# Performance work log

Measured on AMD Instinct MI355X. Metric: run time of the kernel, lower is better.

Reference implementation:

```python
import jax, jax.numpy as jnp
import numpy as np

B, D, H, W = 16, 512, 64, 64
K = 64  # clusters
EPS = 1e-12  # torch F.normalize eps


def _l2norm(v, axis):
    n = jnp.linalg.norm(v, axis=axis, keepdims=True)
    return v / jnp.maximum(n, EPS)


def setup_inputs() -> dict:
    key = jax.random.key(0)
    k1, k2, k3, k4 = jax.random.split(key, 4)
    x = jax.random.normal(k1, (B, D, H, W), dtype=jnp.float32)
    # conv weight/bias are independent trainable params after init; sample them
    centers = jax.random.uniform(k2, (K, D), dtype=jnp.float32)
    conv_w = 2.0 * 100.0 * centers + 0.01 * jax.random.normal(k3, (K, D), dtype=jnp.float32)
    conv_b = -100.0 * jnp.linalg.norm(centers, axis=1) + 0.01 * jax.random.normal(k4, (K,), dtype=jnp.float32)
    return {"x": x, "conv_w": conv_w, "conv_b": conv_b, "centers": centers}


def reference(x, conv_w, conv_b, centers):
    b = x.shape[0]
    x_flat = x.reshape(b, D, -1)                       # (B, D, N)
    # 1x1 conv == per-location linear over channels
    logits = jnp.einsum('bdn,kd->bkn', x_flat, conv_w) + conv_b[None, :, None]
    w = jax.nn.softmax(logits, axis=1)                 # softmax over clusters
    # vlad[b,k,d] = sum_n w[b,k,n]*(x[b,d,n] - c[k,d])
    #            = (w @ x^T)[b,k,d] - (sum_n w[b,k,n]) * c[k,d]
    wx = jnp.einsum('bkn,bdn->bkd', w, x_flat)         # (B, K, D)
    wsum = jnp.sum(w, axis=-1)                          # (B, K)
    vlad = wx - wsum[:, :, None] * centers[None]        # (B, K, D)
    vlad = _l2norm(vlad, axis=2)                        # intra-normalize
    vlad = vlad.reshape(b, -1)
    vlad = _l2norm(vlad, axis=1)                        # global L2
    return vlad
```

## Files before the change

### kernel.cpp

```cpp
#include <hip/hip_runtime.h>
#include <hip/hip_bf16.h>
#include <math.h>

#define B_ 16
#define D_ 512
#define N_ 4096
#define K_ 64

typedef __attribute__((ext_vector_type(8))) short bfrag;
typedef __attribute__((ext_vector_type(4))) float f32x4;

static __device__ __forceinline__ float bf2f(unsigned short u) {
    return __uint_as_float(((unsigned)u) << 16);
}
static __device__ __forceinline__ unsigned short f2bf(float v) {
    __hip_bfloat16 h = __float2bfloat16(v);
    union { __hip_bfloat16 h; unsigned short u; } cv; cv.h = h; return cv.u;
}
static __device__ __forceinline__ void split3(float v, unsigned short& h,
                                              unsigned short& m, unsigned short& l) {
    h = f2bf(v); float r1 = v - bf2f(h);
    m = f2bf(r1); float r2 = r1 - bf2f(m);
    l = f2bf(r2);
}
static __device__ __forceinline__ void split2(float v, unsigned short& h,
                                              unsigned short& l) {
    h = f2bf(v); l = f2bf(v - bf2f(h));
}
#define MFMA(a, b, c) __builtin_amdgcn_mfma_f32_16x16x32_bf16((a), (b), (c), 0, 0, 0)

static __device__ __forceinline__ int xf_idx(int row, int col) {
    const int CH  = col >> 2;
    const int CHs = ((CH - 2 * (row & 7)) & 7) | (CH & 8);
    return row * 68 + CHs * 4 + (col & 3);
}
static __device__ __forceinline__ int ws_idx(int k, int n) {
    const int CH  = n >> 3;
    const int CHs = (CH - 2 * (k & 7)) & 7;
    return k * 72 + CHs * 8 + (n & 7);
}

__global__ __launch_bounds__(256) void k_prep(
    const float* __restrict__ conv_w, unsigned short* __restrict__ cwL)
{
    const int i = blockIdx.x * 256 + threadIdx.x;
    const float4 v = *(const float4*)&conv_w[i * 4];
    const float vv[4] = {v.x, v.y, v.z, v.w};
    unsigned short h[4], m[4], l[4];
    #pragma unroll
    for (int j = 0; j < 4; ++j) split3(vv[j], h[j], m[j], l[j]);
    *(ushort4*)&cwL[0 * (K_ * D_) + i * 4] = make_ushort4(h[0], h[1], h[2], h[3]);
    *(ushort4*)&cwL[1 * (K_ * D_) + i * 4] = make_ushort4(m[0], m[1], m[2], m[3]);
    *(ushort4*)&cwL[2 * (K_ * D_) + i * 4] = make_ushort4(l[0], l[1], l[2], l[3]);
}

__global__ __launch_bounds__(512, 2) void k_fused(
    const float* __restrict__ x, const unsigned short* __restrict__ cwL,
    const float* __restrict__ conv_b, float* __restrict__ vlad_part,
    float* __restrict__ wsumbuf)
{
    const int b    = blockIdx.x >> 4;
    const int g    = blockIdx.x & 15;
    const int tid  = threadIdx.x;
    const int w    = tid >> 6;
    const int lane = tid & 63;
    const int q    = lane >> 4;
    const int c    = lane & 15;
    const int kw   = w >> 1;
    const int nw   = w & 1;
    const int dsub = w * 4;

    extern __shared__ char smem[];
    float*          xf   = (float*)smem;
    unsigned short* xsb  = (unsigned short*)(smem + 139264);
    unsigned short* wsb_ = (unsigned short*)(smem + 139264);
    float*          redm = (float*)(smem + 157696);
    float*          reds = (float*)(smem + 158720);

    f32x4 acc2[16];
    #pragma unroll
    for (int i = 0; i < 16; ++i) acc2[i] = (f32x4){0.f, 0.f, 0.f, 0.f};
    float wacc[4] = {0.f, 0.f, 0.f, 0.f};
    float bias[4];
    #pragma unroll
    for (int r = 0; r < 4; ++r) bias[r] = conv_b[kw * 16 + q * 4 + r];

    const unsigned short* cwp = cwL + (kw * 16 + c) * D_ + q * 8;

    #pragma unroll 1
    for (int t = 0; t < 4; ++t) {
        const int gn0 = g * 256 + t * 64;
        const float* xb = x + (size_t)b * ((size_t)D_ * N_) + gn0 + lane;

        f32x4 accA[2];
        accA[0] = (f32x4){0.f, 0.f, 0.f, 0.f};
        accA[1] = (f32x4){0.f, 0.f, 0.f, 0.f};

        float gx[4];
        #pragma unroll
        for (int r = 0; r < 4; ++r) gx[r] = xb[(size_t)(dsub + r) * N_];

        #pragma unroll 1
        for (int d0 = 0; d0 < D_; d0 += 32) {
            const bfrag af0 = *(const bfrag*)(cwp + d0);
            const bfrag af1 = *(const bfrag*)(cwp + K_ * D_ + d0);
            const bfrag af2 = *(const bfrag*)(cwp + 2 * K_ * D_ + d0);
            const int dn = (d0 + 32) & (D_ - 1);
            float nx[4];
            #pragma unroll
            for (int r = 0; r < 4; ++r) nx[r] = xb[(size_t)(dn + dsub + r) * N_];

            #pragma unroll
            for (int r = 0; r < 4; ++r) xf[xf_idx(d0 + dsub + r, lane)] = gx[r];
            unsigned short h[4], m[4], l[4];
            #pragma unroll
            for (int r = 0; r < 4; ++r) split3(gx[r], h[r], m[r], l[r]);
            {
                const int Cs  = (dsub >> 3) ^ ((lane >> 3) & 3);
                const int dsw = Cs * 8 + (dsub & 7);
                *(ushort4*)&xsb[0 * 2560 + lane * 40 + dsw] = make_ushort4(h[0], h[1], h[2], h[3]);
                *(ushort4*)&xsb[1 * 2560 + lane * 40 + dsw] = make_ushort4(m[0], m[1], m[2], m[3]);
                *(ushort4*)&xsb[2 * 2560 + lane * 40 + dsw] = make_ushort4(l[0], l[1], l[2], l[3]);
            }
            __syncthreads();
            #pragma unroll
            for (int nt = 0; nt < 2; ++nt) {
                const int row = nw * 32 + nt * 16 + c;
                const int qs  = (q ^ ((row >> 3) & 3)) * 8;
                const bfrag bf0 = *(const bfrag*)&xsb[0 * 2560 + row * 40 + qs];
                const bfrag bf1 = *(const bfrag*)&xsb[1 * 2560 + row * 40 + qs];
                const bfrag bf2 = *(const bfrag*)&xsb[2 * 2560 + row * 40 + qs];
                f32x4 a = accA[nt];
                a = MFMA(af0, bf0, a);
                a = MFMA(af0, bf1, a);
                a = MFMA(af1, bf0, a);
                a = MFMA(af1, bf1, a);
                a = MFMA(af0, bf2, a);
                a = MFMA(af2, bf0, a);
                accA[nt] = a;
            }
            __syncthreads();
            #pragma unroll
            for (int r = 0; r < 4; ++r) gx[r] = nx[r];
        }

        #pragma unroll
        for (int nt = 0; nt < 2; ++nt)
            #pragma unroll
            for (int r = 0; r < 4; ++r) accA[nt][r] += bias[r];

        {
            float ml[2];
            #pragma unroll
            for (int nt = 0; nt < 2; ++nt) {
                float mm = fmaxf(fmaxf(accA[nt][0], accA[nt][1]),
                                 fmaxf(accA[nt][2], accA[nt][3]));
                mm = fmaxf(mm, __shfl_xor(mm, 16));
                mm = fmaxf(mm, __shfl_xor(mm, 32));
                ml[nt] = mm;
            }
            if (q == 0) {
                redm[kw * 64 + nw * 32 + c]      = ml[0];
                redm[kw * 64 + nw * 32 + 16 + c] = ml[1];
            }
        }
        __syncthreads();
        float mall[2];
        #pragma unroll
        for (int nt = 0; nt < 2; ++nt) {
            const int n = nw * 32 + nt * 16 + c;
            mall[nt] = fmaxf(fmaxf(redm[n], redm[64 + n]),
                             fmaxf(redm[128 + n], redm[192 + n]));
        }
        float sl[2] = {0.f, 0.f};
        #pragma unroll
        for (int nt = 0; nt < 2; ++nt) {
            #pragma unroll
            for (int r = 0; r < 4; ++r) {
                const float e = __expf(accA[nt][r] - mall[nt]);
                accA[nt][r] = e;
                sl[nt] += e;
            }
            sl[nt] += __shfl_xor(sl[nt], 16);
            sl[nt] += __shfl_xor(sl[nt], 32);
        }
        if (q == 0) {
            reds[kw * 64 + nw * 32 + c]      = sl[0];
            reds[kw * 64 + nw * 32 + 16 + c] = sl[1];
        }
        __syncthreads();
        #pragma unroll
        for (int nt = 0; nt < 2; ++nt) {
            const int n = nw * 32 + nt * 16 + c;
            const float inv = 1.0f / (reds[n] + reds[64 + n] + reds[128 + n] + reds[192 + n]);
            #pragma unroll
            for (int r = 0; r < 4; ++r) {
                const float v = accA[nt][r] * inv;
                unsigned short hi, lo;
                split2(v, hi, lo);
                const int k = kw * 16 + q * 4 + r;
                wsb_[ws_idx(k, n)]        = hi;
                wsb_[4608 + ws_idx(k, n)] = lo;
                wacc[r] += v;
            }
        }
        __syncthreads();

        bfrag awh[2], awl[2];
        #pragma unroll
        for (int ns = 0; ns < 2; ++ns) {
            awh[ns] = *(const bfrag*)&wsb_[ws_idx(kw * 16 + c, ns * 32 + q * 8)];
            awl[ns] = *(const bfrag*)&wsb_[4608 + ws_idx(kw * 16 + c, ns * 32 + q * 8)];
        }
        #pragma unroll
        for (int i = 0; i < 16; ++i) {
            const int row = i * 32 + nw * 16 + c;
            f32x4 a = acc2[i];
            #pragma unroll
            for (int ns = 0; ns < 2; ++ns) {
                const float4 v0 = *(const float4*)&xf[xf_idx(row, ns * 32 + q * 8)];
                const float4 v1 = *(const float4*)&xf[xf_idx(row, ns * 32 + q * 8 + 4)];
                const float vv[8] = {v0.x, v0.y, v0.z, v0.w, v1.x, v1.y, v1.z, v1.w};
                bfrag bh, bl;
                #pragma unroll
                for (int j = 0; j < 8; ++j) {
                    unsigned short hh, ll;
                    split2(vv[j], hh, ll);
                    bh[j] = (short)hh;
                    bl[j] = (short)ll;
                }
                a = MFMA(awh[ns], bh, a);
                a = MFMA(awh[ns], bl, a);
                a = MFMA(awl[ns], bh, a);
            }
            acc2[i] = a;
        }
        __syncthreads();
    }

    #pragma unroll
    for (int msk = 1; msk < 16; msk <<= 1)
        #pragma unroll
        for (int r = 0; r < 4; ++r) wacc[r] += __shfl_xor(wacc[r], msk);
    if (c == 0)
        #pragma unroll
        for (int r = 0; r < 4; ++r)
            atomicAdd(&wsumbuf[b * K_ + kw * 16 + q * 4 + r], wacc[r]);

    float* vp = vlad_part + ((size_t)(b * 16 + g) * K_) * D_;
    #pragma unroll
    for (int i = 0; i < 16; ++i)
        #pragma unroll
        for (int r = 0; r < 4; ++r)
            vp[(size_t)(kw * 16 + q * 4 + r) * D_ + i * 32 + nw * 16 + c] = acc2[i][r];
}

__global__ __launch_bounds__(256) void k_norm(
    const float* __restrict__ wsumbuf, const float* __restrict__ vlad_part,
    const float* __restrict__ centers, float* __restrict__ out)
{
    const int b   = blockIdx.x >> 6;
    const int k   = blockIdx.x & 63;
    const int tid = threadIdx.x;

    const float wsum = wsumbuf[b * K_ + k];

    const float* vp = vlad_part + ((size_t)(b * 16) * K_ + k) * D_;
    float a0 = 0.f, a1 = 0.f;
    #pragma unroll 4
    for (int gg = 0; gg < 16; ++gg) {
        a0 += vp[(size_t)gg * K_ * D_ + tid];
        a1 += vp[(size_t)gg * K_ * D_ + tid + 256];
    }
    const float* cr = centers + k * D_;
    const float v0 = a0 - wsum * cr[tid];
    const float v1 = a1 - wsum * cr[tid + 256];

    float ss = v0 * v0 + v1 * v1;
    __shared__ float red2[4];
    #pragma unroll
    for (int off = 32; off > 0; off >>= 1) ss += __shfl_down(ss, off, 64);
    if ((tid & 63) == 0) red2[tid >> 6] = ss;
    __syncthreads();
    const float nrm = sqrtf(red2[0] + red2[1] + red2[2] + red2[3]);
    const float scale = 1.0f / (8.0f * fmaxf(nrm, 1e-12f));

    float* outr = out + ((size_t)b * K_ + k) * D_;
    outr[tid]       = v0 * scale;
    outr[tid + 256] = v1 * scale;
}

extern "C" void kernel_launch(void* const* d_in, const int* in_sizes, int n_in,
                              void* d_out, int out_size, void* d_ws, size_t ws_size,
                              hipStream_t stream) {
    const float* x       = (const float*)d_in[0];
    const float* conv_w  = (const float*)d_in[1];
    const float* conv_b  = (const float*)d_in[2];
    const float* centers = (const float*)d_in[3];
    float* out = (float*)d_out;

    char* wsp = (char*)d_ws;
    float* vlad_part    = (float*)wsp;
    float* wsumbuf      = (float*)(wsp + (32u << 20));
    unsigned short* cwL = (unsigned short*)(wsp + (32u << 20) + (1u << 16));

    hipMemsetAsync(wsumbuf, 0, B_ * K_ * sizeof(float), stream);

    static bool attr_set = false;
    if (!attr_set) {
        (void)hipFuncSetAttribute((const void*)k_fused,
                                  hipFuncAttributeMaxDynamicSharedMemorySize, 159744);
        attr_set = true;
    }

    k_prep<<<32, 256, 0, stream>>>(conv_w, cwL);
    k_fused<<<B_ * 16, 512, 159744, stream>>>(x, cwL, conv_b, vlad_part, wsumbuf);
    k_norm<<<B_ * K_, 256, 0, stream>>>(wsumbuf, vlad_part, centers, out);
}
```

Before: 257.1 us.

## Halve per-block N tile to double grid size and cut shared memory

Each fused block now handles 128 spatial positions instead of 256, processed in 32-wide chunks, so the grid doubles to 512 blocks and shared memory per block roughly halves. The logits GEMM now steps over 64 channels per iteration, and the LDS layouts and swizzles are rebuilt for the smaller tile. This targets poor CU fill, since 256 blocks cannot cover the machine well, and raises the occupancy hint. The cost is twice as many partial VLAD slabs to write and reduce in the norm kernel, plus more workspace.

After: 352.4 us. 37.1% more time.

```diff
diff --git a/kernel.cpp b/kernel.cpp
--- a/kernel.cpp
+++ b/kernel.cpp
@@ -29,15 +29,8 @@
 }
 #define MFMA(a, b, c) __builtin_amdgcn_mfma_f32_16x16x32_bf16((a), (b), (c), 0, 0, 0)
 
-static __device__ __forceinline__ int xf_idx(int row, int col) {
-    const int CH  = col >> 2;
-    const int CHs = ((CH - 2 * (row & 7)) & 7) | (CH & 8);
-    return row * 68 + CHs * 4 + (col & 3);
-}
-static __device__ __forceinline__ int ws_idx(int k, int n) {
-    const int CH  = n >> 3;
-    const int CHs = (CH - 2 * (k & 7)) & 7;
-    return k * 72 + CHs * 8 + (n & 7);
+static __device__ __forceinline__ int xf_idx(int d, int n) {
+    return d * 32 + ((((n >> 2) - d) & 7) << 2) + (n & 3);
 }
 
 __global__ __launch_bounds__(256) void k_prep(
@@ -54,28 +47,29 @@
     *(ushort4*)&cwL[2 * (K_ * D_) + i * 4] = make_ushort4(l[0], l[1], l[2], l[3]);
 }
 
-__global__ __launch_bounds__(512, 2) void k_fused(
+__global__ __launch_bounds__(512, 4) void k_fused(
     const float* __restrict__ x, const unsigned short* __restrict__ cwL,
     const float* __restrict__ conv_b, float* __restrict__ vlad_part,
     float* __restrict__ wsumbuf)
 {
-    const int b    = blockIdx.x >> 4;
-    const int g    = blockIdx.x & 15;
+    const int b    = blockIdx.x >> 5;
+    const int g    = blockIdx.x & 31;
     const int tid  = threadIdx.x;
     const int w    = tid >> 6;
     const int lane = tid & 63;
     const int q    = lane >> 4;
     const int c    = lane & 15;
     const int kw   = w >> 1;
-    const int nw   = w & 1;
-    const int dsub = w * 4;
+    const int nh   = w & 1;
+    const int sn   = tid & 31;
+    const int sg   = tid >> 5;
 
     extern __shared__ char smem[];
     float*          xf   = (float*)smem;
-    unsigned short* xsb  = (unsigned short*)(smem + 139264);
-    unsigned short* wsb_ = (unsigned short*)(smem + 139264);
-    float*          redm = (float*)(smem + 157696);
-    float*          reds = (float*)(smem + 158720);
+    unsigned short* xsb  = (unsigned short*)(smem + 65536);
+    unsigned short* wsb  = (unsigned short*)(smem + 65536);
+    float*          redm = (float*)(smem + 75776);
+    float*          reds = (float*)(smem + 76288);
 
     f32x4 acc2[16];
     #pragma unroll
@@ -86,58 +80,56 @@
     for (int r = 0; r < 4; ++r) bias[r] = conv_b[kw * 16 + q * 4 + r];
 
     const unsigned short* cwp = cwL + (kw * 16 + c) * D_ + q * 8;
+    const int nloc = nh * 16 + c;
 
     #pragma unroll 1
     for (int t = 0; t < 4; ++t) {
-        const int gn0 = g * 256 + t * 64;
-        const float* xb = x + (size_t)b * ((size_t)D_ * N_) + gn0 + lane;
-
-        f32x4 accA[2];
-        accA[0] = (f32x4){0.f, 0.f, 0.f, 0.f};
-        accA[1] = (f32x4){0.f, 0.f, 0.f, 0.f};
+        const float* xb = x + (size_t)b * ((size_t)D_ * N_) + (g * 128 + t * 32) + sn;
+
+        f32x4 accA = (f32x4){0.f, 0.f, 0.f, 0.f};
 
         float gx[4];
         #pragma unroll
-        for (int r = 0; r < 4; ++r) gx[r] = xb[(size_t)(dsub + r) * N_];
+        for (int r = 0; r < 4; ++r) gx[r] = xb[(size_t)(sg * 4 + r) * N_];
 
         #pragma unroll 1
-        for (int d0 = 0; d0 < D_; d0 += 32) {
-            const bfrag af0 = *(const bfrag*)(cwp + d0);
-            const bfrag af1 = *(const bfrag*)(cwp + K_ * D_ + d0);
-            const bfrag af2 = *(const bfrag*)(cwp + 2 * K_ * D_ + d0);
-            const int dn = (d0 + 32) & (D_ - 1);
+        for (int d0 = 0; d0 < D_; d0 += 64) {
+            bfrag af[2][3];
+            #pragma unroll
+            for (int h = 0; h < 2; ++h)
+                #pragma unroll
+                for (int lv = 0; lv < 3; ++lv)
+                    af[h][lv] = *(const bfrag*)(cwp + lv * (K_ * D_) + d0 + h * 32);
+            const int dn = (d0 + 64) & (D_ - 1);
             float nx[4];
             #pragma unroll
-            for (int r = 0; r < 4; ++r) nx[r] = xb[(size_t)(dn + dsub + r) * N_];
-
-            #pragma unroll
-            for (int r = 0; r < 4; ++r) xf[xf_idx(d0 + dsub + r, lane)] = gx[r];
-            unsigned short h[4], m[4], l[4];
-            #pragma unroll
-            for (int r = 0; r < 4; ++r) split3(gx[r], h[r], m[r], l[r]);
+            for (int r = 0; r < 4; ++r) nx[r] = xb[(size_t)(dn + sg * 4 + r) * N_];
+
+            unsigned short h4[4], m4[4], l4[4];
+            #pragma unroll
+            for (int r = 0; r < 4; ++r) {
+                xf[xf_idx(d0 + sg * 4 + r, sn)] = gx[r];
+                split3(gx[r], h4[r], m4[r], l4[r]);
+            }
             {
-                const int Cs  = (dsub >> 3) ^ ((lane >> 3) & 3);
-                const int dsw = Cs * 8 + (dsub & 7);
-                *(ushort4*)&xsb[0 * 2560 + lane * 40 + dsw] = make_ushort4(h[0], h[1], h[2], h[3]);
-                *(ushort4*)&xsb[1 * 2560 + lane * 40 + dsw] = make_ushort4(m[0], m[1], m[2], m[3]);
-                *(ushort4*)&xsb[2 * 2560 + lane * 40 + dsw] = make_ushort4(l[0], l[1], l[2], l[3]);
+                const int o = sn * 72 + sg * 4;
+                *(ushort4*)&xsb[o]        = make_ushort4(h4[0], h4[1], h4[2], h4[3]);
+                *(ushort4*)&xsb[2304 + o] = make_ushort4(m4[0], m4[1], m4[2], m4[3]);
+                *(ushort4*)&xsb[4608 + o] = make_ushort4(l4[0], l4[1], l4[2], l4[3]);
             }
             __syncthreads();
             #pragma unroll
-            for (int nt = 0; nt < 2; ++nt) {
-                const int row = nw * 32 + nt * 16 + c;
-                const int qs  = (q ^ ((row >> 3) & 3)) * 8;
-                const bfrag bf0 = *(const bfrag*)&xsb[0 * 2560 + row * 40 + qs];
-                const bfrag bf1 = *(const bfrag*)&xsb[1 * 2560 + row * 40 + qs];
-                const bfrag bf2 = *(const bfrag*)&xsb[2 * 2560 + row * 40 + qs];
-                f32x4 a = accA[nt];
-                a = MFMA(af0, bf0, a);
-                a = MFMA(af0, bf1, a);
-                a = MFMA(af1, bf0, a);
-                a = MFMA(af1, bf1, a);
-                a = MFMA(af0, bf2, a);
-                a = MFMA(af2, bf0, a);
-                accA[nt] = a;
+            for (int h = 0; h < 2; ++h) {
+                const int ro = nloc * 72 + h * 32 + q * 8;
+                const bfrag bf0 = *(const bfrag*)&xsb[ro];
+                const bfrag bf1 = *(const bfrag*)&xsb[2304 + ro];
+                const bfrag bf2 = *(const bfrag*)&xsb[4608 + ro];
+                accA = MFMA(af[h][0], bf0, accA);
+                accA = MFMA(af[h][0], bf1, accA);
+                accA = MFMA(af[h][1], bf0, accA);
+                accA = MFMA(af[h][1], bf1, accA);
+                accA = MFMA(af[h][0], bf2, accA);
+                accA = MFMA(af[h][2], bf0, accA);
             }
             __syncthreads();
             #pragma unroll
@@ -145,94 +137,61 @@
         }
 
         #pragma unroll
-        for (int nt = 0; nt < 2; ++nt)
-            #pragma unroll
-            for (int r = 0; r < 4; ++r) accA[nt][r] += bias[r];
-
-        {
-            float ml[2];
-            #pragma unroll
-            for (int nt = 0; nt < 2; ++nt) {
-                float mm = fmaxf(fmaxf(accA[nt][0], accA[nt][1]),
-                                 fmaxf(accA[nt][2], accA[nt][3]));
-                mm = fmaxf(mm, __shfl_xor(mm, 16));
-                mm = fmaxf(mm, __shfl_xor(mm, 32));
-                ml[nt] = mm;
-            }
-            if (q == 0) {
-                redm[kw * 64 + nw * 32 + c]      = ml[0];
-                redm[kw * 64 + nw * 32 + 16 + c] = ml[1];
-            }
-        }
-        __syncthreads();
-        float mall[2];
-        #pragma unroll
-        for (int nt = 0; nt < 2; ++nt) {
-            const int n = nw * 32 + nt * 16 + c;
-            mall[nt] = fmaxf(fmaxf(redm[n], redm[64 + n]),
-                             fmaxf(redm[128 + n], redm[192 + n]));
-        }
-        float sl[2] = {0.f, 0.f};
-        #pragma unroll
-        for (int nt = 0; nt < 2; ++nt) {
-            #pragma unroll
-            for (int r = 0; r < 4; ++r) {
-                const float e = __expf(accA[nt][r] - mall[nt]);
-                accA[nt][r] = e;
-                sl[nt] += e;
-            }
-            sl[nt] += __shfl_xor(sl[nt], 16);
-            sl[nt] += __shfl_xor(sl[nt], 32);
-        }
-        if (q == 0) {
-            reds[kw * 64 + nw * 32 + c]      = sl[0];
-            reds[kw * 64 + nw * 32 + 16 + c] = sl[1];
-        }
-        __syncthreads();
-        #pragma unroll
-        for (int nt = 0; nt < 2; ++nt) {
-            const int n = nw * 32 + nt * 16 + c;
-            const float inv = 1.0f / (reds[n] + reds[64 + n] + reds[128 + n] + reds[192 + n]);
-            #pragma unroll
-            for (int r = 0; r < 4; ++r) {
-                const float v = accA[nt][r] * inv;
-                unsigned short hi, lo;
-                split2(v, hi, lo);
-                const int k = kw * 16 + q * 4 + r;
-                wsb_[ws_idx(k, n)]        = hi;
-                wsb_[4608 + ws_idx(k, n)] = lo;
-                wacc[r] += v;
-            }
-        }
-        __syncthreads();
-
-        bfrag awh[2], awl[2];
-        #pragma unroll
-        for (int ns = 0; ns < 2; ++ns) {
-            awh[ns] = *(const bfrag*)&wsb_[ws_idx(kw * 16 + c, ns * 32 + q * 8)];
-            awl[ns] = *(const bfrag*)&wsb_[4608 + ws_idx(kw * 16 + c, ns * 32 + q * 8)];
-        }
+        for (int r = 0; r < 4; ++r) accA[r] += bias[r];
+
+        float mm = fmaxf(fmaxf(accA[0], accA[1]), fmaxf(accA[2], accA[3]));
+        mm = fmaxf(mm, __shfl_xor(mm, 16));
+        mm = fmaxf(mm, __shfl_xor(mm, 32));
+        if (q == 0) redm[kw * 32 + nloc] = mm;
+        __syncthreads();
+        const float mall = fmaxf(fmaxf(redm[nloc], redm[32 + nloc]),
+                                 fmaxf(redm[64 + nloc], redm[96 + nloc]));
+        float sl = 0.f;
+        #pragma unroll
+        for (int r = 0; r < 4; ++r) {
+            const float e = __expf(accA[r] - mall);
+            accA[r] = e;
+            sl += e;
+        }
+        sl += __shfl_xor(sl, 16);
+        sl += __shfl_xor(sl, 32);
+        if (q == 0) reds[kw * 32 + nloc] = sl;
+        __syncthreads();
+        const float inv = 1.0f / (reds[nloc] + reds[32 + nloc] +
+                                  reds[64 + nloc] + reds[96 + nloc]);
+        #pragma unroll
+        for (int r = 0; r < 4; ++r) {
+            const float v = accA[r] * inv;
+            unsigned short hi, lo;
+            split2(v, hi, lo);
+            const int k = kw * 16 + q * 4 + r;
+            wsb[k * 40 + nloc]        = hi;
+            wsb[2560 + k * 40 + nloc] = lo;
+            wacc[r] += v;
+        }
+        __syncthreads();
+
+        const bfrag awh = *(const bfrag*)&wsb[(kw * 16 + c) * 40 + q * 8];
+        const bfrag awl = *(const bfrag*)&wsb[2560 + (kw * 16 + c) * 40 + q * 8];
         #pragma unroll
         for (int i = 0; i < 16; ++i) {
-            const int row = i * 32 + nw * 16 + c;
+            const int row = i * 32 + nh * 16 + c;
+            const int rb  = row * 32;
+            const float4 v0 = *(const float4*)&xf[rb + (((2 * q     - row) & 7) << 2)];
+            const float4 v1 = *(const float4*)&xf[rb + (((2 * q + 1 - row) & 7) << 2)];
+            const float vv[8] = {v0.x, v0.y, v0.z, v0.w, v1.x, v1.y, v1.z, v1.w};
+            bfrag bh, bl;
+            #pragma unroll
+            for (int j = 0; j < 8; ++j) {
+                unsigned short hh, ll;
+                split2(vv[j], hh, ll);
+                bh[j] = (short)hh;
+                bl[j] = (short)ll;
+            }
             f32x4 a = acc2[i];
-            #pragma unroll
-            for (int ns = 0; ns < 2; ++ns) {
-                const float4 v0 = *(const float4*)&xf[xf_idx(row, ns * 32 + q * 8)];
-                const float4 v1 = *(const float4*)&xf[xf_idx(row, ns * 32 + q * 8 + 4)];
-                const float vv[8] = {v0.x, v0.y, v0.z, v0.w, v1.x, v1.y, v1.z, v1.w};
-                bfrag bh, bl;
-                #pragma unroll
-                for (int j = 0; j < 8; ++j) {
-                    unsigned short hh, ll;
-                    split2(vv[j], hh, ll);
-                    bh[j] = (short)hh;
-                    bl[j] = (short)ll;
-                }
-                a = MFMA(awh[ns], bh, a);
-                a = MFMA(awh[ns], bl, a);
-                a = MFMA(awl[ns], bh, a);
-            }
+            a = MFMA(awh, bh, a);
+            a = MFMA(awh, bl, a);
+            a = MFMA(awl, bh, a);
             acc2[i] = a;
         }
         __syncthreads();
@@ -247,12 +206,12 @@
         for (int r = 0; r < 4; ++r)
             atomicAdd(&wsumbuf[b * K_ + kw * 16 + q * 4 + r], wacc[r]);
 
-    float* vp = vlad_part + ((size_t)(b * 16 + g) * K_) * D_;
+    float* vp = vlad_part + ((size_t)(b * 32 + g) * K_) * D_;
     #pragma unroll
     for (int i = 0; i < 16; ++i)
         #pragma unroll
         for (int r = 0; r < 4; ++r)
-            vp[(size_t)(kw * 16 + q * 4 + r) * D_ + i * 32 + nw * 16 + c] = acc2[i][r];
+            vp[(size_t)(kw * 16 + q * 4 + r) * D_ + i * 32 + nh * 16 + c] = acc2[i][r];
 }
 
 __global__ __launch_bounds__(256) void k_norm(
@@ -265,10 +224,10 @@
 
     const float wsum = wsumbuf[b * K_ + k];
 
-    const float* vp = vlad_part + ((size_t)(b * 16) * K_ + k) * D_;
+    const float* vp = vlad_part + ((size_t)(b * 32) * K_ + k) * D_;
     float a0 = 0.f, a1 = 0.f;
     #pragma unroll 4
-    for (int gg = 0; gg < 16; ++gg) {
+    for (int gg = 0; gg < 32; ++gg) {
         a0 += vp[(size_t)gg * K_ * D_ + tid];
         a1 += vp[(size_t)gg * K_ * D_ + tid + 256];
     }
@@ -301,19 +260,19 @@
 
     char* wsp = (char*)d_ws;
     float* vlad_part    = (float*)wsp;
-    float* wsumbuf      = (float*)(wsp + (32u << 20));
-    unsigned short* cwL = (unsigned short*)(wsp + (32u << 20) + (1u << 16));
+    float* wsumbuf      = (float*)(wsp + (64u << 20));
+    unsigned short* cwL = (unsigned short*)(wsp + (64u << 20) + (1u << 16));
 
     hipMemsetAsync(wsumbuf, 0, B_ * K_ * sizeof(float), stream);
 
     static bool attr_set = false;
     if (!attr_set) {
         (void)hipFuncSetAttribute((const void*)k_fused,
-                                  hipFuncAttributeMaxDynamicSharedMemorySize, 159744);
+                                  hipFuncAttributeMaxDynamicSharedMemorySize, 79360);
         attr_set = true;
     }
 
     k_prep<<<32, 256, 0, stream>>>(conv_w, cwL);
-    k_fused<<<B_ * 16, 512, 159744, stream>>>(x, cwL, conv_b, vlad_part, wsumbuf);
+    k_fused<<<B_ * 32, 512, 79360, stream>>>(x, cwL, conv_b, vlad_part, wsumbuf);
     k_norm<<<B_ * K_, 256, 0, stream>>>(wsumbuf, vlad_part, centers, out);
 }
```

## Store pre-split bf16 x tiles in LDS and software-pipeline the logits loop

Applied to the files above, without the earlier changes.

The fp32 x tile kept in shared memory is replaced by pre-split bf16 high and middle planes, written during the logits pass. The second GEMM now loads ready bfrag operands instead of re-reading fp32 and re-splitting. The logits loop is fully unrolled with double-buffered weight fragments and a 3-deep prefetch of x. __syncthreads is replaced by explicit lgkmcnt waits plus raw s_barrier with sched_barriers. The intent is to cut VALU split work and LDS traffic and to hide global latency, at the cost of more registers and a new unswizzled LDS layout that may cause bank conflicts.

After: 307.7 us. 19.7% more time.

```diff
diff --git a/kernel.cpp b/kernel.cpp
--- a/kernel.cpp
+++ b/kernel.cpp
@@ -29,11 +29,6 @@
 }
 #define MFMA(a, b, c) __builtin_amdgcn_mfma_f32_16x16x32_bf16((a), (b), (c), 0, 0, 0)
 
-static __device__ __forceinline__ int xf_idx(int row, int col) {
-    const int CH  = col >> 2;
-    const int CHs = ((CH - 2 * (row & 7)) & 7) | (CH & 8);
-    return row * 68 + CHs * 4 + (col & 3);
-}
 static __device__ __forceinline__ int ws_idx(int k, int n) {
     const int CH  = n >> 3;
     const int CHs = (CH - 2 * (k & 7)) & 7;
@@ -71,9 +66,10 @@
     const int dsub = w * 4;
 
     extern __shared__ char smem[];
-    float*          xf   = (float*)smem;
+    unsigned short* Lh   = (unsigned short*)smem;
+    unsigned short* Lm   = (unsigned short*)(smem + 69632);
     unsigned short* xsb  = (unsigned short*)(smem + 139264);
-    unsigned short* wsb_ = (unsigned short*)(smem + 139264);
+    unsigned short* wsb  = (unsigned short*)(smem + 139264);
     float*          redm = (float*)(smem + 157696);
     float*          reds = (float*)(smem + 158720);
 
@@ -96,33 +92,50 @@
         accA[0] = (f32x4){0.f, 0.f, 0.f, 0.f};
         accA[1] = (f32x4){0.f, 0.f, 0.f, 0.f};
 
-        float gx[4];
-        #pragma unroll
-        for (int r = 0; r < 4; ++r) gx[r] = xb[(size_t)(dsub + r) * N_];
-
-        #pragma unroll 1
-        for (int d0 = 0; d0 < D_; d0 += 32) {
-            const bfrag af0 = *(const bfrag*)(cwp + d0);
-            const bfrag af1 = *(const bfrag*)(cwp + K_ * D_ + d0);
-            const bfrag af2 = *(const bfrag*)(cwp + 2 * K_ * D_ + d0);
-            const int dn = (d0 + 32) & (D_ - 1);
-            float nx[4];
-            #pragma unroll
-            for (int r = 0; r < 4; ++r) nx[r] = xb[(size_t)(dn + dsub + r) * N_];
-
-            #pragma unroll
-            for (int r = 0; r < 4; ++r) xf[xf_idx(d0 + dsub + r, lane)] = gx[r];
-            unsigned short h[4], m[4], l[4];
-            #pragma unroll
-            for (int r = 0; r < 4; ++r) split3(gx[r], h[r], m[r], l[r]);
+        float gxb[3][4];
+        bfrag afb[2][3];
+
+        #pragma unroll
+        for (int r = 0; r < 4; ++r) gxb[0][r] = xb[(size_t)(dsub + r) * N_];
+        #pragma unroll
+        for (int lv = 0; lv < 3; ++lv)
+            afb[0][lv] = *(const bfrag*)(cwp + lv * (K_ * D_));
+        #pragma unroll
+        for (int r = 0; r < 4; ++r) gxb[1][r] = xb[(size_t)(32 + dsub + r) * N_];
+
+        #pragma unroll
+        for (int s = 0; s < 16; ++s) {
+            const int d0 = s * 32;
+            if (s < 15) {
+                #pragma unroll
+                for (int lv = 0; lv < 3; ++lv)
+                    afb[(s + 1) & 1][lv] =
+                        *(const bfrag*)(cwp + lv * (K_ * D_) + (s + 1) * 32);
+            }
+            if (s < 14) {
+                #pragma unroll
+                for (int r = 0; r < 4; ++r)
+                    gxb[(s + 2) % 3][r] =
+                        xb[(size_t)((s + 2) * 32 + dsub + r) * N_];
+            }
+            unsigned short h4[4], m4[4], l4[4];
+            #pragma unroll
+            for (int r = 0; r < 4; ++r) {
+                split3(gxb[s % 3][r], h4[r], m4[r], l4[r]);
+                Lh[(d0 + dsub + r) * 68 + lane] = h4[r];
+                Lm[(d0 + dsub + r) * 68 + lane] = m4[r];
+            }
             {
                 const int Cs  = (dsub >> 3) ^ ((lane >> 3) & 3);
                 const int dsw = Cs * 8 + (dsub & 7);
-                *(ushort4*)&xsb[0 * 2560 + lane * 40 + dsw] = make_ushort4(h[0], h[1], h[2], h[3]);
-                *(ushort4*)&xsb[1 * 2560 + lane * 40 + dsw] = make_ushort4(m[0], m[1], m[2], m[3]);
-                *(ushort4*)&xsb[2 * 2560 + lane * 40 + dsw] = make_ushort4(l[0], l[1], l[2], l[3]);
-            }
-            __syncthreads();
+                *(ushort4*)&xsb[0 * 2560 + lane * 40 + dsw] = make_ushort4(h4[0], h4[1], h4[2], h4[3]);
+                *(ushort4*)&xsb[1 * 2560 + lane * 40 + dsw] = make_ushort4(m4[0], m4[1], m4[2], m4[3]);
+                *(ushort4*)&xsb[2 * 2560 + lane * 40 + dsw] = make_ushort4(l4[0], l4[1], l4[2], l4[3]);
+            }
+            asm volatile("s_waitcnt lgkmcnt(0)" ::: "memory");
+            __builtin_amdgcn_sched_barrier(0);
+            __builtin_amdgcn_s_barrier();
+            __builtin_amdgcn_sched_barrier(0);
             #pragma unroll
             for (int nt = 0; nt < 2; ++nt) {
                 const int row = nw * 32 + nt * 16 + c;
@@ -131,17 +144,18 @@
                 const bfrag bf1 = *(const bfrag*)&xsb[1 * 2560 + row * 40 + qs];
                 const bfrag bf2 = *(const bfrag*)&xsb[2 * 2560 + row * 40 + qs];
                 f32x4 a = accA[nt];
-                a = MFMA(af0, bf0, a);
-                a = MFMA(af0, bf1, a);
-                a = MFMA(af1, bf0, a);
-                a = MFMA(af1, bf1, a);
-                a = MFMA(af0, bf2, a);
-                a = MFMA(af2, bf0, a);
+                a = MFMA(afb[s & 1][0], bf0, a);
+                a = MFMA(afb[s & 1][0], bf1, a);
+                a = MFMA(afb[s & 1][1], bf0, a);
+                a = MFMA(afb[s & 1][1], bf1, a);
+                a = MFMA(afb[s & 1][0], bf2, a);
+                a = MFMA(afb[s & 1][2], bf0, a);
                 accA[nt] = a;
             }
-            __syncthreads();
-            #pragma unroll
-            for (int r = 0; r < 4; ++r) gx[r] = nx[r];
+            asm volatile("s_waitcnt lgkmcnt(0)" ::: "memory");
+            __builtin_amdgcn_sched_barrier(0);
+            __builtin_amdgcn_s_barrier();
+            __builtin_amdgcn_sched_barrier(0);
         }
 
         #pragma unroll
@@ -199,8 +213,8 @@
                 unsigned short hi, lo;
                 split2(v, hi, lo);
                 const int k = kw * 16 + q * 4 + r;
-                wsb_[ws_idx(k, n)]        = hi;
-                wsb_[4608 + ws_idx(k, n)] = lo;
+                wsb[ws_idx(k, n)]        = hi;
+                wsb[4608 + ws_idx(k, n)] = lo;
                 wacc[r] += v;
             }
         }
@@ -209,8 +223,8 @@
         bfrag awh[2], awl[2];
         #pragma unroll
         for (int ns = 0; ns < 2; ++ns) {
-            awh[ns] = *(const bfrag*)&wsb_[ws_idx(kw * 16 + c, ns * 32 + q * 8)];
-            awl[ns] = *(const bfrag*)&wsb_[4608 + ws_idx(kw * 16 + c, ns * 32 + q * 8)];
+            awh[ns] = *(const bfrag*)&wsb[ws_idx(kw * 16 + c, ns * 32 + q * 8)];
+            awl[ns] = *(const bfrag*)&wsb[4608 + ws_idx(kw * 16 + c, ns * 32 + q * 8)];
         }
         #pragma unroll
         for (int i = 0; i < 16; ++i) {
@@ -218,17 +232,8 @@
             f32x4 a = acc2[i];
             #pragma unroll
             for (int ns = 0; ns < 2; ++ns) {
-                const float4 v0 = *(const float4*)&xf[xf_idx(row, ns * 32 + q * 8)];
-                const float4 v1 = *(const float4*)&xf[xf_idx(row, ns * 32 + q * 8 + 4)];
-                const float vv[8] = {v0.x, v0.y, v0.z, v0.w, v1.x, v1.y, v1.z, v1.w};
-                bfrag bh, bl;
-                #pragma unroll
-                for (int j = 0; j < 8; ++j) {
-                    unsigned short hh, ll;
-                    split2(vv[j], hh, ll);
-                    bh[j] = (short)hh;
-                    bl[j] = (short)ll;
-                }
+                const bfrag bh = *(const bfrag*)&Lh[row * 68 + ns * 32 + q * 8];
+                const bfrag bl = *(const bfrag*)&Lm[row * 68 + ns * 32 + q * 8];
                 a = MFMA(awh[ns], bh, a);
                 a = MFMA(awh[ns], bl, a);
                 a = MFMA(awl[ns], bh, a);
```
